# Optimization experiments

Measured on AMD Instinct MI355X. Metric: run time of the kernel, lower is better.

The kernel has to match this reference:

```python
import jax, jax.numpy as jnp
import numpy as np

B, S, D, H = 4, 1024, 1024, 16
HD = D // H
EPS = 1e-5


def setup_inputs() -> dict:
    key = jax.random.key(0)
    ks = jax.random.split(key, 12)
    sc = 0.02
    return {
        "x": jax.random.normal(ks[0], (B, S, D), jnp.float32),
        "WQ": jax.random.normal(ks[1], (D, D), jnp.float32) * sc,
        "WK": jax.random.normal(ks[2], (D, D), jnp.float32) * sc,
        "WV": jax.random.normal(ks[3], (D, D), jnp.float32) * sc,
        "Wo": jax.random.normal(ks[4], (D, D), jnp.float32) * sc,
        "bo": jnp.zeros((D,), jnp.float32),
        "W1": jax.random.normal(ks[5], (D, 4 * D), jnp.float32) * sc,
        "b1": jnp.zeros((4 * D,), jnp.float32),
        "W2": jax.random.normal(ks[6], (4 * D, D), jnp.float32) * sc,
        "b2": jnp.zeros((D,), jnp.float32),
        "ln1_s": jnp.ones((D,), jnp.float32),
        "ln1_b": jnp.zeros((D,), jnp.float32),
        "ln2_s": jnp.ones((D,), jnp.float32),
        "ln2_b": jnp.zeros((D,), jnp.float32),
    }


def _layernorm(x, scale, shift):
    mean = jnp.mean(x, axis=-1, keepdims=True)
    var = jnp.mean((x - mean) ** 2, axis=-1, keepdims=True)  # unbiased=False
    return scale * ((x - mean) / jnp.sqrt(var + EPS)) + shift


def _gelu(x):
    c = jnp.sqrt(2.0 / jnp.pi).astype(x.dtype)
    return 0.5 * x * (1.0 + jnp.tanh(c * (x + 0.044715 * x ** 3)))


def reference(x, WQ, WK, WV, Wo, bo, W1, b1, W2, b2, ln1_s, ln1_b, ln2_s, ln2_b):
    b, s, d = x.shape
    # --- attention sub-block (pre-norm) ---
    h = _layernorm(x, ln1_s, ln1_b)
    q = (h @ WQ).reshape(b, s, H, HD).transpose(0, 2, 1, 3)  # [B,H,S,HD]
    k = (h @ WK).reshape(b, s, H, HD).transpose(0, 2, 1, 3)
    v = (h @ WV).reshape(b, s, H, HD).transpose(0, 2, 1, 3)
    scores = jnp.einsum("bhqd,bhkd->bhqk", q, k)
    causal = jnp.triu(jnp.ones((s, s), dtype=bool), k=1)
    scores = jnp.where(causal, -jnp.inf, scores)
    attn = jax.nn.softmax(scores / jnp.sqrt(jnp.float32(HD)), axis=-1)
    ctx = jnp.einsum("bhqk,bhkd->bhqd", attn, v)
    ctx = ctx.transpose(0, 2, 1, 3).reshape(b, s, d)
    x = x + (ctx @ Wo + bo)
    # --- FF sub-block (pre-norm) ---
    h = _layernorm(x, ln2_s, ln2_b)
    h = _gelu(h @ W1 + b1)
    return x + (h @ W2 + b2)
```

## Files before the change

### kernel.cpp

```cpp
#include <hip/hip_runtime.h>
#include <hip/hip_bf16.h>

#define DIM   1024
#define NHEAD 16
#define HDIM  64
#define BATCH 4
#define SEQ   1024
#define MTOT  (BATCH*SEQ)
#define DFF   (4*DIM)
#define LDQ   3072

typedef _Float16 f16x8 __attribute__((ext_vector_type(8)));
typedef _Float16 f16x4 __attribute__((ext_vector_type(4)));
typedef float    f32x4 __attribute__((ext_vector_type(4)));

__device__ __forceinline__ float geluf(float x) {
    float z2 = 1.5957691216057308f * (x + 0.044715f * x * x * x);
    return x * __builtin_amdgcn_rcpf(1.0f + __expf(-z2));
}

__device__ __forceinline__ int swz_off(int row, int slot) {
    return row * 128 + ((slot ^ (row & 7)) << 4);
}
__device__ __forceinline__ f16x8 ldsfrag(const _Float16* s, int row, int slot) {
    return *(const f16x8*)((const char*)s + swz_off(row, slot));
}

template <int NCHUNK>
__device__ __forceinline__ void stage_async(const _Float16* __restrict__ g, int ld,
                                            _Float16* s, int w, int lane) {
    int r_in = lane >> 3;
    int sslot = lane & 7;
    int lslot = sslot ^ r_in;
#pragma unroll
    for (int q = 0; q < NCHUNK; ++q) {
        int chunk = w * NCHUNK + q;
        int row = chunk * 8 + r_in;
        const _Float16* gp = g + (size_t)row * ld + lslot * 8;
        _Float16* sp = s + chunk * 512;
        __builtin_amdgcn_global_load_lds(
            (const __attribute__((address_space(1))) void*)gp,
            (__attribute__((address_space(3))) void*)sp, 16, 0, 0);
    }
}

__global__ __launch_bounds__(256) void k_tcvt(const float* __restrict__ src,
                                              _Float16* __restrict__ dst,
                                              int K, int N) {
    __shared__ float tile[32][33];
    int n0 = blockIdx.x * 32, k0 = blockIdx.y * 32;
    int tx = threadIdx.x, ty = threadIdx.y;
#pragma unroll
    for (int i = 0; i < 32; i += 8)
        tile[ty + i][tx] = src[(size_t)(k0 + ty + i) * N + (n0 + tx)];
    __syncthreads();
#pragma unroll
    for (int i = 0; i < 32; i += 8)
        dst[(size_t)(n0 + ty + i) * K + (k0 + tx)] = (_Float16)tile[tx][ty + i];
}

__global__ __launch_bounds__(256) void k_tcvt4(const float* __restrict__ s0,
                                               const float* __restrict__ s1,
                                               const float* __restrict__ s2,
                                               const float* __restrict__ s3,
                                               _Float16* __restrict__ dst) {
    __shared__ float tile[32][33];
    const float* src = blockIdx.z == 0 ? s0 : (blockIdx.z == 1 ? s1 :
                       (blockIdx.z == 2 ? s2 : s3));
    _Float16* d = dst + (size_t)blockIdx.z * (1024 * 1024);
    int n0 = blockIdx.x * 32, k0 = blockIdx.y * 32;
    int tx = threadIdx.x, ty = threadIdx.y;
#pragma unroll
    for (int i = 0; i < 32; i += 8)
        tile[ty + i][tx] = src[(size_t)(k0 + ty + i) * 1024 + (n0 + tx)];
    __syncthreads();
#pragma unroll
    for (int i = 0; i < 32; i += 8)
        d[(size_t)(n0 + ty + i) * 1024 + (k0 + tx)] = (_Float16)tile[tx][ty + i];
}

__global__ __launch_bounds__(256) void k_ln(const float* __restrict__ x,
                                            const float* __restrict__ sc,
                                            const float* __restrict__ sh,
                                            _Float16* __restrict__ out) {
    int row = blockIdx.x;
    int t = threadIdx.x;
    float4 v = ((const float4*)(x + (size_t)row * DIM))[t];
    float sum = v.x + v.y + v.z + v.w;
    float sq  = v.x * v.x + v.y * v.y + v.z * v.z + v.w * v.w;
#pragma unroll
    for (int m = 1; m < 64; m <<= 1) {
        sum += __shfl_xor(sum, m);
        sq  += __shfl_xor(sq, m);
    }
    __shared__ float rs[4], rq[4];
    int w = t >> 6;
    if ((t & 63) == 0) { rs[w] = sum; rq[w] = sq; }
    __syncthreads();
    sum = rs[0] + rs[1] + rs[2] + rs[3];
    sq  = rq[0] + rq[1] + rq[2] + rq[3];
    float mean = sum * (1.0f / DIM);
    float var  = sq * (1.0f / DIM) - mean * mean;
    float rstd = rsqrtf(var + 1e-5f);
    float4 s4 = ((const float4*)sc)[t];
    float4 b4 = ((const float4*)sh)[t];
    f16x4 o;
    o[0] = (_Float16)(s4.x * ((v.x - mean) * rstd) + b4.x);
    o[1] = (_Float16)(s4.y * ((v.y - mean) * rstd) + b4.y);
    o[2] = (_Float16)(s4.z * ((v.z - mean) * rstd) + b4.z);
    o[3] = (_Float16)(s4.w * ((v.w - mean) * rstd) + b4.w);
    ((f16x4*)(out + (size_t)row * DIM))[t] = o;
}

template <int EPI>
__global__ __launch_bounds__(256) void k_gemm(const _Float16* __restrict__ A,
                                              const _Float16* __restrict__ BT,
                                              int N, int K, int gx,
                                              _Float16* __restrict__ Ch,
                                              const float* __restrict__ bias) {
    __shared__ _Float16 As[2][128 * 64];
    __shared__ _Float16 Bs[2][128 * 64];
    int t = threadIdx.x;
    int bid = blockIdx.x;
    int lin = (bid & 7) * ((int)gridDim.x >> 3) + (bid >> 3);
    int m0 = (lin / gx) * 128, n0 = (lin % gx) * 128;
    int lane = t & 63, w = t >> 6;
    int wm = (w >> 1) * 64, wn = (w & 1) * 64;
    int lr = lane & 15, lg = lane >> 4;
    f32x4 acc[4][4];
#pragma unroll
    for (int i = 0; i < 4; ++i)
#pragma unroll
        for (int j = 0; j < 4; ++j) acc[i][j] = (f32x4){0.f, 0.f, 0.f, 0.f};

    const _Float16* Ag = A  + (size_t)m0 * K;
    const _Float16* Bg = BT + (size_t)n0 * K;
    int nt = K / 64;
    stage_async<4>(Ag, K, As[0], w, lane);
    stage_async<4>(Bg, K, Bs[0], w, lane);
    for (int tt = 0; tt < nt; ++tt) {
        int cur = tt & 1, nxt = cur ^ 1;
        if (tt + 1 < nt) {
            stage_async<4>(Ag + (tt + 1) * 64, K, As[nxt], w, lane);
            stage_async<4>(Bg + (tt + 1) * 64, K, Bs[nxt], w, lane);
            asm volatile("s_waitcnt vmcnt(8)" ::: "memory");
        } else {
            asm volatile("s_waitcnt vmcnt(0)" ::: "memory");
        }
        __builtin_amdgcn_sched_barrier(0);
        __builtin_amdgcn_s_barrier();
        __builtin_amdgcn_sched_barrier(0);
#pragma unroll
        for (int kk = 0; kk < 2; ++kk) {
            f16x8 a[4], b[4];
#pragma unroll
            for (int i = 0; i < 4; ++i) a[i] = ldsfrag(As[cur], wm + i * 16 + lr, kk * 4 + lg);
#pragma unroll
            for (int j = 0; j < 4; ++j) b[j] = ldsfrag(Bs[cur], wn + j * 16 + lr, kk * 4 + lg);
            __builtin_amdgcn_s_setprio(1);
#pragma unroll
            for (int i = 0; i < 4; ++i)
#pragma unroll
                for (int j = 0; j < 4; ++j)
                    acc[i][j] = __builtin_amdgcn_mfma_f32_16x16x32_f16(a[i], b[j], acc[i][j], 0, 0, 0);
            __builtin_amdgcn_s_setprio(0);
        }
        __builtin_amdgcn_s_barrier();
    }
#pragma unroll
    for (int i = 0; i < 4; ++i) {
#pragma unroll
        for (int j = 0; j < 4; ++j) {
            int row = m0 + wm + i * 16 + lg * 4;
            int col = n0 + wn + j * 16 + lr;
#pragma unroll
            for (int r = 0; r < 4; ++r) {
                float v = acc[i][j][r];
                size_t idx = (size_t)(row + r) * N + col;
                if constexpr (EPI == 0) Ch[idx] = (_Float16)v;
                else                    Ch[idx] = (_Float16)geluf(v + bias[col]);
            }
        }
    }
}

__global__ __launch_bounds__(256) void k_gemm64(const _Float16* __restrict__ A,
                                                const _Float16* __restrict__ BT,
                                                int N, int K,
                                                float* __restrict__ Cf,
                                                const float* __restrict__ bias,
                                                const float* __restrict__ resid) {
    __shared__ _Float16 As[3][128 * 64];
    __shared__ _Float16 Bs[3][64 * 64];
    int t = threadIdx.x;
    int bid = blockIdx.x;
    int lin = (bid & 7) * ((int)gridDim.x >> 3) + (bid >> 3);
    int gx = N / 64;
    int m0 = (lin / gx) * 128, n0 = (lin % gx) * 64;
    int lane = t & 63, w = t >> 6;
    int wm = w * 32;
    int lr = lane & 15, lg = lane >> 4;
    f32x4 acc[2][4];
#pragma unroll
    for (int i = 0; i < 2; ++i)
#pragma unroll
        for (int j = 0; j < 4; ++j) acc[i][j] = (f32x4){0.f, 0.f, 0.f, 0.f};

    const _Float16* Ag = A  + (size_t)m0 * K;
    const _Float16* Bg = BT + (size_t)n0 * K;
    int nt = K / 64;
    stage_async<4>(Ag, K, As[0], w, lane);
    stage_async<2>(Bg, K, Bs[0], w, lane);
    stage_async<4>(Ag + 64, K, As[1], w, lane);
    stage_async<2>(Bg + 64, K, Bs[1], w, lane);
    for (int tt = 0; tt < nt; ++tt) {
        if (tt + 1 < nt) asm volatile("s_waitcnt vmcnt(6)" ::: "memory");
        else             asm volatile("s_waitcnt vmcnt(0)" ::: "memory");
        __builtin_amdgcn_sched_barrier(0);
        __builtin_amdgcn_s_barrier();
        __builtin_amdgcn_sched_barrier(0);
        if (tt + 2 < nt) {
            int nb = (tt + 2) % 3;
            stage_async<4>(Ag + (tt + 2) * 64, K, As[nb], w, lane);
            stage_async<2>(Bg + (tt + 2) * 64, K, Bs[nb], w, lane);
        }
        const _Float16* Ac = As[tt % 3];
        const _Float16* Bc = Bs[tt % 3];
#pragma unroll
        for (int kk = 0; kk < 2; ++kk) {
            f16x8 a[2], b[4];
#pragma unroll
            for (int i = 0; i < 2; ++i) a[i] = ldsfrag(Ac, wm + i * 16 + lr, kk * 4 + lg);
#pragma unroll
            for (int j = 0; j < 4; ++j) b[j] = ldsfrag(Bc, j * 16 + lr, kk * 4 + lg);
            __builtin_amdgcn_s_setprio(1);
#pragma unroll
            for (int i = 0; i < 2; ++i)
#pragma unroll
                for (int j = 0; j < 4; ++j)
                    acc[i][j] = __builtin_amdgcn_mfma_f32_16x16x32_f16(a[i], b[j], acc[i][j], 0, 0, 0);
            __builtin_amdgcn_s_setprio(0);
        }
    }
#pragma unroll
    for (int i = 0; i < 2; ++i) {
#pragma unroll
        for (int j = 0; j < 4; ++j) {
            int row = m0 + wm + i * 16 + lg * 4;
            int col = n0 + j * 16 + lr;
#pragma unroll
            for (int r = 0; r < 4; ++r) {
                size_t idx = (size_t)(row + r) * N + col;
                Cf[idx] = acc[i][j][r] + bias[col] + resid[idx];
            }
        }
    }
}

__global__ __launch_bounds__(64) void k_attn(const _Float16* __restrict__ QKV,
                                             _Float16* __restrict__ Og) {
    __shared__ _Float16 Ps[32 * 64];
    int lane = threadIdx.x;
    int id = blockIdx.x;
    int bh = id & 63;
    int qt = (SEQ / 32 - 1) - (id >> 6);
    int h = bh & 15, b = bh >> 4;
    int q0 = qt * 32;
    int lr = lane & 15, lg = lane >> 4;
    size_t base = (size_t)b * SEQ;
    int cq = h * HDIM, ck = 1024 + h * HDIM, cv = 2048 + h * HDIM;

    f16x8 aq[2][2];
#pragma unroll
    for (int i = 0; i < 2; ++i)
#pragma unroll
        for (int kk = 0; kk < 2; ++kk) {
            f16x8 v = *(const f16x8*)(QKV + (base + q0 + i * 16 + lr) * LDQ + cq + kk * 32 + lg * 8);
#pragma unroll
            for (int e = 0; e < 8; ++e) v[e] = v[e] * (_Float16)0.125f;
            aq[i][kk] = v;
        }

    f32x4 cacc[2][4];
#pragma unroll
    for (int i = 0; i < 2; ++i)
#pragma unroll
        for (int j = 0; j < 4; ++j) cacc[i][j] = (f32x4){0.f, 0.f, 0.f, 0.f};
    float mrun[2], lrun[2];
#pragma unroll
    for (int i = 0; i < 2; ++i) { mrun[i] = -1e30f; lrun[i] = 0.f; }

    int ntiles = q0 / 64 + 1;
    for (int kt = 0; kt < ntiles; ++kt) {
        int k0 = kt * 64;
        f32x4 sacc[2][4];
#pragma unroll
        for (int i = 0; i < 2; ++i)
#pragma unroll
            for (int j = 0; j < 4; ++j) sacc[i][j] = (f32x4){0.f, 0.f, 0.f, 0.f};
#pragma unroll
        for (int kk = 0; kk < 2; ++kk) {
            f16x8 bk[4];
#pragma unroll
            for (int j = 0; j < 4; ++j)
                bk[j] = *(const f16x8*)(QKV + (base + k0 + j * 16 + lr) * LDQ + ck + kk * 32 + lg * 8);
            __builtin_amdgcn_s_setprio(1);
#pragma unroll
            for (int i = 0; i < 2; ++i)
#pragma unroll
                for (int j = 0; j < 4; ++j)
                    sacc[i][j] = __builtin_amdgcn_mfma_f32_16x16x32_f16(bk[j], aq[i][kk], sacc[i][j], 0, 0, 0);
            __builtin_amdgcn_s_setprio(0);
        }
        if (kt == ntiles - 1) {
#pragma unroll
            for (int i = 0; i < 2; ++i) {
                int qq = q0 + i * 16 + lr;
#pragma unroll
                for (int j = 0; j < 4; ++j)
#pragma unroll
                    for (int r = 0; r < 4; ++r) {
                        int kc = k0 + j * 16 + lg * 4 + r;
                        if (kc > qq) sacc[i][j][r] = -1e30f;
                    }
            }
        }
#pragma unroll
        for (int i = 0; i < 2; ++i) {
            float tm = -1e30f;
#pragma unroll
            for (int j = 0; j < 4; ++j)
#pragma unroll
                for (int r = 0; r < 4; ++r) tm = fmaxf(tm, sacc[i][j][r]);
            tm = fmaxf(tm, __shfl_xor(tm, 16));
            tm = fmaxf(tm, __shfl_xor(tm, 32));
            float m2 = fmaxf(mrun[i], tm);
            float al = __expf(mrun[i] - m2);
            mrun[i] = m2;
#pragma unroll
            for (int jd = 0; jd < 4; ++jd)
#pragma unroll
                for (int r = 0; r < 4; ++r) cacc[i][jd][r] *= al;
            float ps = 0.f;
#pragma unroll
            for (int j = 0; j < 4; ++j)
#pragma unroll
                for (int r = 0; r < 4; ++r) {
                    float p = __expf(sacc[i][j][r] - m2);
                    sacc[i][j][r] = p;
                    ps += p;
                }
            ps += __shfl_xor(ps, 16);
            ps += __shfl_xor(ps, 32);
            lrun[i] = lrun[i] * al + ps;
        }
#pragma unroll
        for (int i = 0; i < 2; ++i) {
            int q = i * 16 + lr;
#pragma unroll
            for (int j = 0; j < 4; ++j) {
                int kc0 = j * 16 + lg * 4;
                int ks = kc0 >> 3;
                f16x4 pv4;
#pragma unroll
                for (int r = 0; r < 4; ++r) pv4[r] = (_Float16)sacc[i][j][r];
                *(f16x4*)((char*)Ps + q * 128 + ((ks ^ (q & 7)) << 4) + (kc0 & 7) * 2) = pv4;
            }
        }
        {
            const _Float16* vb = QKV + (base + k0) * LDQ + cv;
#pragma unroll
            for (int kk = 0; kk < 2; ++kk) {
                f16x8 pa[2], bv[4];
#pragma unroll
                for (int i = 0; i < 2; ++i) pa[i] = ldsfrag(Ps, i * 16 + lr, kk * 4 + lg);
                const _Float16* vk = vb + (size_t)(kk * 32 + lg * 8) * LDQ + lr;
#pragma unroll
                for (int jd = 0; jd < 4; ++jd)
#pragma unroll
                    for (int e = 0; e < 8; ++e)
                        bv[jd][e] = vk[(size_t)e * LDQ + jd * 16];
                __builtin_amdgcn_s_setprio(1);
#pragma unroll
                for (int i = 0; i < 2; ++i)
#pragma unroll
                    for (int jd = 0; jd < 4; ++jd)
                        cacc[i][jd] = __builtin_amdgcn_mfma_f32_16x16x32_f16(bv[jd], pa[i], cacc[i][jd], 0, 0, 0);
                __builtin_amdgcn_s_setprio(0);
            }
        }
    }
#pragma unroll
    for (int i = 0; i < 2; ++i) {
        float rl = 1.0f / lrun[i];
        int qq = q0 + i * 16 + lr;
#pragma unroll
        for (int jd = 0; jd < 4; ++jd) {
            f16x4 o4;
#pragma unroll
            for (int r = 0; r < 4; ++r) o4[r] = (_Float16)(cacc[i][jd][r] * rl);
            *(f16x4*)(Og + (base + qq) * DIM + h * HDIM + jd * 16 + lg * 4) = o4;
        }
    }
}

extern "C" void kernel_launch(void* const* d_in, const int* in_sizes, int n_in,
                              void* d_out, int out_size, void* d_ws, size_t ws_size,
                              hipStream_t stream) {
    const float* x    = (const float*)d_in[0];
    const float* WQ   = (const float*)d_in[1];
    const float* WK   = (const float*)d_in[2];
    const float* WV   = (const float*)d_in[3];
    const float* Wo   = (const float*)d_in[4];
    const float* bo   = (const float*)d_in[5];
    const float* W1   = (const float*)d_in[6];
    const float* b1   = (const float*)d_in[7];
    const float* W2   = (const float*)d_in[8];
    const float* b2   = (const float*)d_in[9];
    const float* ln1s = (const float*)d_in[10];
    const float* ln1b = (const float*)d_in[11];
    const float* ln2s = (const float*)d_in[12];
    const float* ln2b = (const float*)d_in[13];
    float* out = (float*)d_out;
    char* ws = (char*)d_ws;
    const size_t MB = 1024 * 1024;
    _Float16* WTqkv = (_Float16*)(ws + 0 * MB);
    _Float16* WTo   = (_Float16*)(ws + 6 * MB);
    _Float16* WT1   = (_Float16*)(ws + 8 * MB);
    _Float16* WT2   = (_Float16*)(ws + 16 * MB);
    _Float16* h1    = (_Float16*)(ws + 24 * MB);
    _Float16* qkvb  = (_Float16*)(ws + 32 * MB);
    _Float16* ctx   = (_Float16*)(ws + 56 * MB);
    _Float16* h2    = (_Float16*)(ws + 64 * MB);
    _Float16* ff1   = (_Float16*)(ws + 72 * MB);
    float*    x2    = (float*)   (ws + 104 * MB);

    dim3 tb(32, 8);
    k_tcvt4<<<dim3(32, 32, 4), tb, 0, stream>>>(WQ, WK, WV, Wo, WTqkv);
    k_tcvt<<<dim3(128, 32), tb, 0, stream>>>(W1, WT1, 1024, 4096);
    k_tcvt<<<dim3(32, 128), tb, 0, stream>>>(W2, WT2, 4096, 1024);

    k_ln<<<MTOT, 256, 0, stream>>>(x, ln1s, ln1b, h1);

    k_gemm<0><<<dim3(768), 256, 0, stream>>>(h1, WTqkv, LDQ, DIM, 24, qkvb, nullptr);

    k_attn<<<dim3(2048), 64, 0, stream>>>(qkvb, ctx);

    k_gemm64<<<dim3(512), 256, 0, stream>>>(ctx, WTo, DIM, DIM, x2, bo, x);

    k_ln<<<MTOT, 256, 0, stream>>>(x2, ln2s, ln2b, h2);

    k_gemm<1><<<dim3(1024), 256, 0, stream>>>(h2, WT1, DFF, DIM, 32, ff1, b1);

    k_gemm64<<<dim3(512), 256, 0, stream>>>(ff1, WT2, DIM, DFF, out, b2, x2);
}
```

Baseline: 235.1 us.

## Load A operands directly into registers in k_gemm64, staging only B in LDS

Measured after the change: 250.8 us. 1.07x slower.

```diff
diff --git a/kernel.cpp b/kernel.cpp
--- a/kernel.cpp
+++ b/kernel.cpp
@@ -184,13 +184,53 @@
     }
 }
 
+__device__ __forceinline__ void load_a_regs(const _Float16* __restrict__ Ag, int K,
+                                            int koff, int wm, int lr, int lg,
+                                            f16x8 (&ar)[2][2]) {
+#pragma unroll
+    for (int i = 0; i < 2; ++i)
+#pragma unroll
+        for (int kk = 0; kk < 2; ++kk)
+            ar[i][kk] = *(const f16x8*)(Ag + (size_t)(wm + i * 16 + lr) * K + koff + kk * 32 + lg * 8);
+}
+
+__device__ __forceinline__ void g64_step(int u, int nt,
+                                         const _Float16* __restrict__ Ag,
+                                         const _Float16* __restrict__ Bg, int K,
+                                         _Float16 (*Bs)[64 * 64],
+                                         f16x8 (&AR)[2][2], f32x4 (&acc)[2][4],
+                                         int w, int lane, int wm, int lr, int lg) {
+    if (u + 1 < nt) asm volatile("s_waitcnt vmcnt(6)" ::: "memory");
+    else            asm volatile("s_waitcnt vmcnt(0)" ::: "memory");
+    __builtin_amdgcn_sched_barrier(0);
+    __builtin_amdgcn_s_barrier();
+    __builtin_amdgcn_sched_barrier(0);
+    const _Float16* Bc = Bs[u % 3];
+#pragma unroll
+    for (int kk = 0; kk < 2; ++kk) {
+        f16x8 b[4];
+#pragma unroll
+        for (int j = 0; j < 4; ++j) b[j] = ldsfrag(Bc, j * 16 + lr, kk * 4 + lg);
+        __builtin_amdgcn_s_setprio(1);
+#pragma unroll
+        for (int i = 0; i < 2; ++i)
+#pragma unroll
+            for (int j = 0; j < 4; ++j)
+                acc[i][j] = __builtin_amdgcn_mfma_f32_16x16x32_f16(AR[i][kk], b[j], acc[i][j], 0, 0, 0);
+        __builtin_amdgcn_s_setprio(0);
+    }
+    if (u + 2 < nt) {
+        load_a_regs(Ag, K, (u + 2) * 64, wm, lr, lg, AR);
+        stage_async<2>(Bg + (u + 2) * 64, K, Bs[(u + 2) % 3], w, lane);
+    }
+}
+
 __global__ __launch_bounds__(256) void k_gemm64(const _Float16* __restrict__ A,
                                                 const _Float16* __restrict__ BT,
                                                 int N, int K,
                                                 float* __restrict__ Cf,
                                                 const float* __restrict__ bias,
                                                 const float* __restrict__ resid) {
-    __shared__ _Float16 As[3][128 * 64];
     __shared__ _Float16 Bs[3][64 * 64];
     int t = threadIdx.x;
     int bid = blockIdx.x;
@@ -209,38 +249,14 @@
     const _Float16* Ag = A  + (size_t)m0 * K;
     const _Float16* Bg = BT + (size_t)n0 * K;
     int nt = K / 64;
-    stage_async<4>(Ag, K, As[0], w, lane);
+    f16x8 aA[2][2], aB[2][2];
+    load_a_regs(Ag, K, 0, wm, lr, lg, aA);
     stage_async<2>(Bg, K, Bs[0], w, lane);
-    stage_async<4>(Ag + 64, K, As[1], w, lane);
+    load_a_regs(Ag, K, 64, wm, lr, lg, aB);
     stage_async<2>(Bg + 64, K, Bs[1], w, lane);
-    for (int tt = 0; tt < nt; ++tt) {
-        if (tt + 1 < nt) asm volatile("s_waitcnt vmcnt(6)" ::: "memory");
-        else             asm volatile("s_waitcnt vmcnt(0)" ::: "memory");
-        __builtin_amdgcn_sched_barrier(0);
-        __builtin_amdgcn_s_barrier();
-        __builtin_amdgcn_sched_barrier(0);
-        if (tt + 2 < nt) {
-            int nb = (tt + 2) % 3;
-            stage_async<4>(Ag + (tt + 2) * 64, K, As[nb], w, lane);
-            stage_async<2>(Bg + (tt + 2) * 64, K, Bs[nb], w, lane);
-        }
-        const _Float16* Ac = As[tt % 3];
-        const _Float16* Bc = Bs[tt % 3];
-#pragma unroll
-        for (int kk = 0; kk < 2; ++kk) {
-            f16x8 a[2], b[4];
-#pragma unroll
-            for (int i = 0; i < 2; ++i) a[i] = ldsfrag(Ac, wm + i * 16 + lr, kk * 4 + lg);
-#pragma unroll
-            for (int j = 0; j < 4; ++j) b[j] = ldsfrag(Bc, j * 16 + lr, kk * 4 + lg);
-            __builtin_amdgcn_s_setprio(1);
-#pragma unroll
-            for (int i = 0; i < 2; ++i)
-#pragma unroll
-                for (int j = 0; j < 4; ++j)
-                    acc[i][j] = __builtin_amdgcn_mfma_f32_16x16x32_f16(a[i], b[j], acc[i][j], 0, 0, 0);
-            __builtin_amdgcn_s_setprio(0);
-        }
+    for (int tt = 0; tt < nt; tt += 2) {
+        g64_step(tt,     nt, Ag, Bg, K, Bs, aA, acc, w, lane, wm, lr, lg);
+        g64_step(tt + 1, nt, Ag, Bg, K, Bs, aB, acc, w, lane, wm, lr, lg);
     }
 #pragma unroll
     for (int i = 0; i < 2; ++i) {
```

## Prefetch next K tile in attention and reorder GEMM async staging after MFMA

Applied to the files above, without the earlier changes.

Result: faster. 218.5 us, median of 3 (-7.1%).

```diff
diff --git a/kernel.cpp b/kernel.cpp
--- a/kernel.cpp
+++ b/kernel.cpp
@@ -219,28 +219,28 @@
         __builtin_amdgcn_sched_barrier(0);
         __builtin_amdgcn_s_barrier();
         __builtin_amdgcn_sched_barrier(0);
+        const _Float16* Ac = As[tt % 3];
+        const _Float16* Bc = Bs[tt % 3];
+#pragma unroll
+        for (int kk = 0; kk < 2; ++kk) {
+            f16x8 a[2], b[4];
+#pragma unroll
+            for (int i = 0; i < 2; ++i) a[i] = ldsfrag(Ac, wm + i * 16 + lr, kk * 4 + lg);
+#pragma unroll
+            for (int j = 0; j < 4; ++j) b[j] = ldsfrag(Bc, j * 16 + lr, kk * 4 + lg);
+            __builtin_amdgcn_s_setprio(1);
+#pragma unroll
+            for (int i = 0; i < 2; ++i)
+#pragma unroll
+                for (int j = 0; j < 4; ++j)
+                    acc[i][j] = __builtin_amdgcn_mfma_f32_16x16x32_f16(a[i], b[j], acc[i][j], 0, 0, 0);
+            __builtin_amdgcn_s_setprio(0);
+        }
         if (tt + 2 < nt) {
             int nb = (tt + 2) % 3;
             stage_async<4>(Ag + (tt + 2) * 64, K, As[nb], w, lane);
             stage_async<2>(Bg + (tt + 2) * 64, K, Bs[nb], w, lane);
         }
-        const _Float16* Ac = As[tt % 3];
-        const _Float16* Bc = Bs[tt % 3];
-#pragma unroll
-        for (int kk = 0; kk < 2; ++kk) {
-            f16x8 a[2], b[4];
-#pragma unroll
-            for (int i = 0; i < 2; ++i) a[i] = ldsfrag(Ac, wm + i * 16 + lr, kk * 4 + lg);
-#pragma unroll
-            for (int j = 0; j < 4; ++j) b[j] = ldsfrag(Bc, j * 16 + lr, kk * 4 + lg);
-            __builtin_amdgcn_s_setprio(1);
-#pragma unroll
-            for (int i = 0; i < 2; ++i)
-#pragma unroll
-                for (int j = 0; j < 4; ++j)
-                    acc[i][j] = __builtin_amdgcn_mfma_f32_16x16x32_f16(a[i], b[j], acc[i][j], 0, 0, 0);
-            __builtin_amdgcn_s_setprio(0);
-        }
     }
 #pragma unroll
     for (int i = 0; i < 2; ++i) {
@@ -254,6 +254,118 @@
                 Cf[idx] = acc[i][j][r] + bias[col] + resid[idx];
             }
         }
+    }
+}
+
+__device__ __forceinline__ void load_k(const _Float16* __restrict__ QKV,
+                                       size_t base, int k0, int ck,
+                                       int lr, int lg, f16x8 (&kr)[2][4]) {
+#pragma unroll
+    for (int kk = 0; kk < 2; ++kk)
+#pragma unroll
+        for (int j = 0; j < 4; ++j)
+            kr[kk][j] = *(const f16x8*)(QKV + (base + k0 + j * 16 + lr) * LDQ + ck + kk * 32 + lg * 8);
+}
+
+__device__ __forceinline__ void attn_tile_sw(const _Float16* __restrict__ QKV,
+                                             const f16x8 (&bk)[2][4],
+                                             f16x8 (&knext)[2][4], bool pf, int k0next,
+                                             const f16x8 (&aq)[2][2],
+                                             f32x4 (&cacc)[2][4],
+                                             float (&mrun)[2], float (&lrun)[2],
+                                             _Float16* Ps,
+                                             size_t base, int ck, int cv,
+                                             int k0, int q0, bool diag,
+                                             int lr, int lg) {
+    f32x4 sacc[2][4];
+#pragma unroll
+    for (int i = 0; i < 2; ++i)
+#pragma unroll
+        for (int j = 0; j < 4; ++j) sacc[i][j] = (f32x4){0.f, 0.f, 0.f, 0.f};
+    __builtin_amdgcn_s_setprio(1);
+#pragma unroll
+    for (int kk = 0; kk < 2; ++kk)
+#pragma unroll
+        for (int i = 0; i < 2; ++i)
+#pragma unroll
+            for (int j = 0; j < 4; ++j)
+                sacc[i][j] = __builtin_amdgcn_mfma_f32_16x16x32_f16(bk[kk][j], aq[i][kk], sacc[i][j], 0, 0, 0);
+    __builtin_amdgcn_s_setprio(0);
+    if (pf) load_k(QKV, base, k0next, ck, lr, lg, knext);
+    if (diag) {
+#pragma unroll
+        for (int i = 0; i < 2; ++i) {
+            int qq = q0 + i * 16 + lr;
+#pragma unroll
+            for (int j = 0; j < 4; ++j)
+#pragma unroll
+                for (int r = 0; r < 4; ++r) {
+                    int kc = k0 + j * 16 + lg * 4 + r;
+                    if (kc > qq) sacc[i][j][r] = -1e30f;
+                }
+        }
+    }
+#pragma unroll
+    for (int i = 0; i < 2; ++i) {
+        float tm = -1e30f;
+#pragma unroll
+        for (int j = 0; j < 4; ++j)
+#pragma unroll
+            for (int r = 0; r < 4; ++r) tm = fmaxf(tm, sacc[i][j][r]);
+        tm = fmaxf(tm, __shfl_xor(tm, 16));
+        tm = fmaxf(tm, __shfl_xor(tm, 32));
+        float m2 = fmaxf(mrun[i], tm);
+        float al = __expf(mrun[i] - m2);
+        mrun[i] = m2;
+#pragma unroll
+        for (int jd = 0; jd < 4; ++jd)
+#pragma unroll
+            for (int r = 0; r < 4; ++r) cacc[i][jd][r] *= al;
+        float ps = 0.f;
+#pragma unroll
+        for (int j = 0; j < 4; ++j)
+#pragma unroll
+            for (int r = 0; r < 4; ++r) {
+                float p = __expf(sacc[i][j][r] - m2);
+                sacc[i][j][r] = p;
+                ps += p;
+            }
+        ps += __shfl_xor(ps, 16);
+        ps += __shfl_xor(ps, 32);
+        lrun[i] = lrun[i] * al + ps;
+    }
+#pragma unroll
+    for (int i = 0; i < 2; ++i) {
+        int q = i * 16 + lr;
+#pragma unroll
+        for (int j = 0; j < 4; ++j) {
+            int kc0 = j * 16 + lg * 4;
+            int ks = kc0 >> 3;
+            f16x4 pv4;
+#pragma unroll
+            for (int r = 0; r < 4; ++r) pv4[r] = (_Float16)sacc[i][j][r];
+            *(f16x4*)((char*)Ps + q * 128 + ((ks ^ (q & 7)) << 4) + (kc0 & 7) * 2) = pv4;
+        }
+    }
+    const _Float16* vb = QKV + (base + k0) * LDQ + cv;
+#pragma unroll
+    for (int kk = 0; kk < 2; ++kk) {
+        f16x8 pa[2], bv[4];
+#pragma unroll
+        for (int i = 0; i < 2; ++i) pa[i] = ldsfrag(Ps, i * 16 + lr, kk * 4 + lg);
+        const _Float16* vk = vb + (size_t)(kk * 32 + lg * 8) * LDQ + lr;
+#pragma unroll
+        for (int jd = 0; jd < 4; ++jd)
+#pragma unroll
+            for (int e = 0; e < 8; ++e)
+                bv[jd][e] = vk[(size_t)e * LDQ + jd * 16];
+        __builtin_amdgcn_s_setprio(1);
+#pragma unroll
+        for (int i = 0; i < 2; ++i)
+#pragma unroll
+            for (int jd = 0; jd < 4; ++jd)
+                cacc[i][jd] = __builtin_amdgcn_mfma_f32_16x16x32_f16(bv[jd], pa[i], cacc[i][jd], 0, 0, 0);
+        __builtin_amdgcn_s_setprio(0);
     }
 }
 
@@ -291,104 +403,16 @@
     for (int i = 0; i < 2; ++i) { mrun[i] = -1e30f; lrun[i] = 0.f; }
 
     int ntiles = q0 / 64 + 1;
-    for (int kt = 0; kt < ntiles; ++kt) {
-        int k0 = kt * 64;
-        f32x4 sacc[2][4];
-#pragma unroll
-        for (int i = 0; i < 2; ++i)
-#pragma unroll
-            for (int j = 0; j < 4; ++j) sacc[i][j] = (f32x4){0.f, 0.f, 0.f, 0.f};
-#pragma unroll
-        for (int kk = 0; kk < 2; ++kk) {
-            f16x8 bk[4];
-#pragma unroll
-            for (int j = 0; j < 4; ++j)
-                bk[j] = *(const f16x8*)(QKV + (base + k0 + j * 16 + lr) * LDQ + ck + kk * 32 + lg * 8);
-            __builtin_amdgcn_s_setprio(1);
-#pragma unroll
-            for (int i = 0; i < 2; ++i)
-#pragma unroll
-                for (int j = 0; j < 4; ++j)
-                    sacc[i][j] = __builtin_amdgcn_mfma_f32_16x16x32_f16(bk[j], aq[i][kk], sacc[i][j], 0, 0, 0);
-            __builtin_amdgcn_s_setprio(0);
-        }
-        if (kt == ntiles - 1) {
-#pragma unroll
-            for (int i = 0; i < 2; ++i) {
-                int qq = q0 + i * 16 + lr;
-#pragma unroll
-                for (int j = 0; j < 4; ++j)
-#pragma unroll
-                    for (int r = 0; r < 4; ++r) {
-                        int kc = k0 + j * 16 + lg * 4 + r;
-                        if (kc > qq) sacc[i][j][r] = -1e30f;
-                    }
-            }
-        }
-#pragma unroll
-        for (int i = 0; i < 2; ++i) {
-            float tm = -1e30f;
-#pragma unroll
-            for (int j = 0; j < 4; ++j)
-#pragma unroll
-                for (int r = 0; r < 4; ++r) tm = fmaxf(tm, sacc[i][j][r]);
-            tm = fmaxf(tm, __shfl_xor(tm, 16));
-            tm = fmaxf(tm, __shfl_xor(tm, 32));
-            float m2 = fmaxf(mrun[i], tm);
-            float al = __expf(mrun[i] - m2);
-            mrun[i] = m2;
-#pragma unroll
-            for (int jd = 0; jd < 4; ++jd)
-#pragma unroll
-                for (int r = 0; r < 4; ++r) cacc[i][jd][r] *= al;
-            float ps = 0.f;
-#pragma unroll
-            for (int j = 0; j < 4; ++j)
-#pragma unroll
-                for (int r = 0; r < 4; ++r) {
-                    float p = __expf(sacc[i][j][r] - m2);
-                    sacc[i][j][r] = p;
-                    ps += p;
-                }
-            ps += __shfl_xor(ps, 16);
-            ps += __shfl_xor(ps, 32);
-            lrun[i] = lrun[i] * al + ps;
-        }
-#pragma unroll
-        for (int i = 0; i < 2; ++i) {
-            int q = i * 16 + lr;
-#pragma unroll
-            for (int j = 0; j < 4; ++j) {
-                int kc0 = j * 16 + lg * 4;
-                int ks = kc0 >> 3;
-                f16x4 pv4;
-#pragma unroll
-                for (int r = 0; r < 4; ++r) pv4[r] = (_Float16)sacc[i][j][r];
-                *(f16x4*)((char*)Ps + q * 128 + ((ks ^ (q & 7)) << 4) + (kc0 & 7) * 2) = pv4;
-            }
-        }
-        {
-            const _Float16* vb = QKV + (base + k0) * LDQ + cv;
-#pragma unroll
-            for (int kk = 0; kk < 2; ++kk) {
-                f16x8 pa[2], bv[4];
-#pragma unroll
-                for (int i = 0; i < 2; ++i) pa[i] = ldsfrag(Ps, i * 16 + lr, kk * 4 + lg);
-                const _Float16* vk = vb + (size_t)(kk * 32 + lg * 8) * LDQ + lr;
-#pragma unroll
-                for (int jd = 0; jd < 4; ++jd)
-#pragma unroll
-                    for (int e = 0; e < 8; ++e)
-                        bv[jd][e] = vk[(size_t)e * LDQ + jd * 16];
-                __builtin_amdgcn_s_setprio(1);
-#pragma unroll
-                for (int i = 0; i < 2; ++i)
-#pragma unroll
-                    for (int jd = 0; jd < 4; ++jd)
-                        cacc[i][jd] = __builtin_amdgcn_mfma_f32_16x16x32_f16(bv[jd], pa[i], cacc[i][jd], 0, 0, 0);
-                __builtin_amdgcn_s_setprio(0);
-            }
-        }
+    f16x8 kA[2][4], kB[2][4];
+    load_k(QKV, base, 0, ck, lr, lg, kA);
+    for (int kt = 0; kt < ntiles; kt += 2) {
+        attn_tile_sw(QKV, kA, kB, kt + 1 < ntiles, (kt + 1) * 64,
+                     aq, cacc, mrun, lrun, Ps, base, ck, cv,
+                     kt * 64, q0, kt == ntiles - 1, lr, lg);
+        if (kt + 1 >= ntiles) break;
+        attn_tile_sw(QKV, kB, kA, kt + 2 < ntiles, (kt + 2) * 64,
+                     aq, cacc, mrun, lrun, Ps, base, ck, cv,
+                     (kt + 1) * 64, q0, kt + 1 == ntiles - 1, lr, lg);
     }
 #pragma unroll
     for (int i = 0; i < 2; ++i) {
```
